# Kernel tuning notes

Measured on AMD Instinct MI355X. Metric: run time of the kernel, lower is better.

## Reference

```python
import jax, jax.numpy as jnp
import numpy as np

H = 1024        # hidden_size
V = 50257       # output_size (vocab)
L = 50          # max_length (encoder positions)
N_LAYERS = 2    # python loop count over the shared single-layer GRU


def setup_inputs() -> dict:
    key = jax.random.key(0)
    ks = jax.random.split(key, 16)
    s = 0.02
    return {
        "input_ids": jax.random.randint(ks[0], (1,), 0, V),
        "hidden": jax.random.normal(ks[1], (1, 1, H), jnp.float32),
        "encoder_outputs": jax.random.normal(ks[2], (L, H), jnp.float32),
        # learned parameters
        "emb": jax.random.normal(ks[3], (V, H), jnp.float32) * s,
        "attn_w": jax.random.normal(ks[4], (L, 2 * H), jnp.float32) * s,
        "attn_b": jnp.zeros((L,), jnp.float32),
        "comb_w": jax.random.normal(ks[5], (H, 2 * H), jnp.float32) * s,
        "comb_b": jnp.zeros((H,), jnp.float32),
        "w_ih": jax.random.normal(ks[6], (3 * H, H), jnp.float32) * s,
        "w_hh": jax.random.normal(ks[7], (3 * H, H), jnp.float32) * s,
        "b_ih": jnp.zeros((3 * H,), jnp.float32),
        "b_hh": jnp.zeros((3 * H,), jnp.float32),
        "out_w": jax.random.normal(ks[8], (V, H), jnp.float32) * s,
        "out_b": jnp.zeros((V,), jnp.float32),
    }


def _gru_cell(x, h, w_ih, w_hh, b_ih, b_hh):
    # PyTorch GRU gate order: [r, z, n] stacked along dim 0 of (3H, H) weights.
    gx = w_ih @ x + b_ih
    gh = w_hh @ h + b_hh
    r = jax.nn.sigmoid(gx[:H] + gh[:H])
    z = jax.nn.sigmoid(gx[H:2 * H] + gh[H:2 * H])
    n = jnp.tanh(gx[2 * H:] + r * gh[2 * H:])
    return (1.0 - z) * n + z * h


def reference(input_ids, hidden, encoder_outputs, emb, attn_w, attn_b,
              comb_w, comb_b, w_ih, w_hh, b_ih, b_hh, out_w, out_b):
    # batch=1 single decode step; dropout is identity (eval mode)
    embedded = emb[input_ids[0]]                     # [H]
    h = hidden[0, 0]                                 # [H]
    concat = jnp.concatenate([embedded, h])          # [2H]
    attn_weights = jax.nn.softmax(attn_w @ concat + attn_b)   # [L]
    attn_applied = attn_weights @ encoder_outputs    # [H]  (bmm with batch 1)
    output = comb_w @ jnp.concatenate([embedded, attn_applied]) + comb_b  # [H]
    for _ in range(N_LAYERS):                        # shared-weight GRU called twice
        x = jax.nn.relu(output)
        h = _gru_cell(x, h, w_ih, w_hh, b_ih, b_hh)
        output = h
    log_probs = jax.nn.log_softmax(out_w @ output + out_b)    # [V]
    return log_probs[None, :], h[None, None, :], attn_weights[None, :]
```

## Files before the change

kernel.cpp:

```cpp
#include <hip/hip_runtime.h>
#include <hip/hip_bf16.h>

#define H 1024
#define V 50257
#define L 50

__global__ void attn_kernel(const int* __restrict__ input_ids,
                            const float* __restrict__ hidden,
                            const float* __restrict__ enc,
                            const float* __restrict__ emb,
                            const float* __restrict__ attn_w,
                            const float* __restrict__ attn_b,
                            float* __restrict__ ws_emb,
                            float* __restrict__ ws_app,
                            float* __restrict__ out_attnw) {
    __shared__ __align__(16) float s_concat[2 * H];
    __shared__ float s_w[L];
    const int tid = threadIdx.x;
    const int token = input_ids[0];

    const float4* e4 = (const float4*)(emb + (size_t)token * H);
    const float4* h4 = (const float4*)hidden;
    {
        float4 e = e4[tid];
        float4 h = h4[tid];
        ((float4*)s_concat)[tid] = e;
        ((float4*)(s_concat + H))[tid] = h;
        ((float4*)ws_emb)[tid] = e;
    }
    __syncthreads();

    const int wave = tid >> 6, lane = tid & 63;
    for (int l = wave; l < L; l += 4) {
        const float4* r4 = (const float4*)(attn_w + (size_t)l * 2 * H);
        const float4* c4 = (const float4*)s_concat;
        float acc = 0.f;
        for (int k = lane; k < 512; k += 64) {
            float4 a = r4[k], b = c4[k];
            acc += a.x * b.x + a.y * b.y + a.z * b.z + a.w * b.w;
        }
        #pragma unroll
        for (int off = 32; off; off >>= 1) acc += __shfl_down(acc, off);
        if (lane == 0) s_w[l] = acc + attn_b[l];
    }
    __syncthreads();

    if (tid == 0) {
        float m = s_w[0];
        for (int l = 1; l < L; ++l) m = fmaxf(m, s_w[l]);
        float s = 0.f;
        for (int l = 0; l < L; ++l) { s_w[l] = __expf(s_w[l] - m); s += s_w[l]; }
        float inv = 1.f / s;
        for (int l = 0; l < L; ++l) s_w[l] *= inv;
    }
    __syncthreads();
    if (tid < L) out_attnw[tid] = s_w[tid];

    float4 acc = make_float4(0.f, 0.f, 0.f, 0.f);
    for (int l = 0; l < L; ++l) {
        float w = s_w[l];
        float4 v = ((const float4*)(enc + (size_t)l * H))[tid];
        acc.x += w * v.x; acc.y += w * v.y; acc.z += w * v.z; acc.w += w * v.w;
    }
    ((float4*)ws_app)[tid] = acc;
}

__global__ void comb_kernel(const float* __restrict__ comb_w,
                            const float* __restrict__ comb_b,
                            const float* __restrict__ embedded,
                            const float* __restrict__ applied,
                            float* __restrict__ x1) {
    __shared__ __align__(16) float s_c[2 * H];
    const int tid = threadIdx.x;
    ((float4*)s_c)[tid] = ((const float4*)embedded)[tid];
    ((float4*)(s_c + H))[tid] = ((const float4*)applied)[tid];
    __syncthreads();

    const int wave = tid >> 6, lane = tid & 63;
    const int i = blockIdx.x * 4 + wave;
    const float4* r4 = (const float4*)(comb_w + (size_t)i * 2 * H);
    const float4* c4 = (const float4*)s_c;
    float acc = 0.f;
    for (int k = lane; k < 512; k += 64) {
        float4 a = r4[k], b = c4[k];
        acc += a.x * b.x + a.y * b.y + a.z * b.z + a.w * b.w;
    }
    #pragma unroll
    for (int off = 32; off; off >>= 1) acc += __shfl_down(acc, off);
    if (lane == 0) x1[i] = fmaxf(acc + comb_b[i], 0.f);
}

__global__ void gru_kernel(const float* __restrict__ x,
                           const float* __restrict__ hprev,
                           const float* __restrict__ w_ih,
                           const float* __restrict__ w_hh,
                           const float* __restrict__ b_ih,
                           const float* __restrict__ b_hh,
                           float* __restrict__ h_out,
                           float* __restrict__ x_out,
                           float* __restrict__ h_copy)
{
    __shared__ __align__(16) float s_x[H];
    __shared__ __align__(16) float s_h[H];
    const int tid = threadIdx.x;
    ((float4*)s_x)[tid] = ((const float4*)x)[tid];
    ((float4*)s_h)[tid] = ((const float4*)hprev)[tid];
    __syncthreads();

    const int wave = tid >> 6, lane = tid & 63;
    const int i = blockIdx.x * 4 + wave;
    const float4* x4 = (const float4*)s_x;
    const float4* h4 = (const float4*)s_h;
    const float4* wr_x = (const float4*)(w_ih + (size_t)i * H);
    const float4* wz_x = (const float4*)(w_ih + (size_t)(H + i) * H);
    const float4* wn_x = (const float4*)(w_ih + (size_t)(2 * H + i) * H);
    const float4* wr_h = (const float4*)(w_hh + (size_t)i * H);
    const float4* wz_h = (const float4*)(w_hh + (size_t)(H + i) * H);
    const float4* wn_h = (const float4*)(w_hh + (size_t)(2 * H + i) * H);

    float ar = 0.f, az = 0.f, an = 0.f, br = 0.f, bz = 0.f, bn = 0.f;
    for (int k = lane; k < 256; k += 64) {
        float4 xv = x4[k], hv = h4[k], t;
        t = wr_x[k]; ar += t.x * xv.x + t.y * xv.y + t.z * xv.z + t.w * xv.w;
        t = wz_x[k]; az += t.x * xv.x + t.y * xv.y + t.z * xv.z + t.w * xv.w;
        t = wn_x[k]; an += t.x * xv.x + t.y * xv.y + t.z * xv.z + t.w * xv.w;
        t = wr_h[k]; br += t.x * hv.x + t.y * hv.y + t.z * hv.z + t.w * hv.w;
        t = wz_h[k]; bz += t.x * hv.x + t.y * hv.y + t.z * hv.z + t.w * hv.w;
        t = wn_h[k]; bn += t.x * hv.x + t.y * hv.y + t.z * hv.z + t.w * hv.w;
    }
    #pragma unroll
    for (int off = 32; off; off >>= 1) {
        ar += __shfl_down(ar, off); az += __shfl_down(az, off);
        an += __shfl_down(an, off); br += __shfl_down(br, off);
        bz += __shfl_down(bz, off); bn += __shfl_down(bn, off);
    }
    if (lane == 0) {
        float gxr = ar + b_ih[i],         ghr = br + b_hh[i];
        float gxz = az + b_ih[H + i],     ghz = bz + b_hh[H + i];
        float gxn = an + b_ih[2 * H + i], ghn = bn + b_hh[2 * H + i];
        float r = 1.f / (1.f + expf(-(gxr + ghr)));
        float z = 1.f / (1.f + expf(-(gxz + ghz)));
        float n = tanhf(gxn + r * ghn);
        float hn = (1.f - z) * n + z * s_h[i];
        h_out[i] = hn;
        if (x_out) x_out[i] = fmaxf(hn, 0.f);
        if (h_copy) h_copy[i] = hn;
    }
}

__global__ void logits_kernel(const float* __restrict__ out_w,
                              const float* __restrict__ out_b,
                              const float* __restrict__ h,
                              float* __restrict__ logits,
                              float* __restrict__ partials) {
    __shared__ __align__(16) float s_h[H];
    __shared__ float s_part[4];
    const int tid = threadIdx.x;
    ((float4*)s_h)[tid] = ((const float4*)h)[tid];
    __syncthreads();

    const int wave = tid >> 6, lane = tid & 63;
    const float4* h4 = (const float4*)s_h;
    float psum = 0.f;
    #pragma unroll
    for (int rr = 0; rr < 2; ++rr) {
        const int v = blockIdx.x * 8 + wave * 2 + rr;
        if (v < V) {
            const float4* w4 = (const float4*)(out_w + (size_t)v * H);
            float acc = 0.f;
            for (int k = lane; k < 256; k += 64) {
                float4 a = w4[k], b = h4[k];
                acc += a.x * b.x + a.y * b.y + a.z * b.z + a.w * b.w;
            }
            #pragma unroll
            for (int off = 32; off; off >>= 1) acc += __shfl_down(acc, off);
            if (lane == 0) {
                float lg = acc + out_b[v];
                logits[v] = lg;
                psum += expf(lg);
            }
        }
    }
    if (lane == 0) s_part[wave] = psum;
    __syncthreads();
    if (tid == 0) partials[blockIdx.x] = s_part[0] + s_part[1] + s_part[2] + s_part[3];
}

__global__ void lse_kernel(const float* __restrict__ partials, int n,
                           float* __restrict__ lse) {
    __shared__ float red[256];
    const int tid = threadIdx.x;
    float s = 0.f;
    for (int i = tid; i < n; i += 256) s += partials[i];
    red[tid] = s;
    __syncthreads();
    for (int off = 128; off; off >>= 1) {
        if (tid < off) red[tid] += red[tid + off];
        __syncthreads();
    }
    if (tid == 0) *lse = logf(red[0]);
}

__global__ void sub_kernel(const float* __restrict__ logits,
                           const float* __restrict__ lse,
                           float* __restrict__ out) {
    const int v = blockIdx.x * 256 + threadIdx.x;
    if (v < V) out[v] = logits[v] - *lse;
}

extern "C" void kernel_launch(void* const* d_in, const int* in_sizes, int n_in,
                              void* d_out, int out_size, void* d_ws, size_t ws_size,
                              hipStream_t stream) {
    const int*   input_ids = (const int*)d_in[0];
    const float* hidden    = (const float*)d_in[1];
    const float* enc       = (const float*)d_in[2];
    const float* emb       = (const float*)d_in[3];
    const float* attn_w    = (const float*)d_in[4];
    const float* attn_b    = (const float*)d_in[5];
    const float* comb_w    = (const float*)d_in[6];
    const float* comb_b    = (const float*)d_in[7];
    const float* w_ih      = (const float*)d_in[8];
    const float* w_hh      = (const float*)d_in[9];
    const float* b_ih      = (const float*)d_in[10];
    const float* b_hh      = (const float*)d_in[11];
    const float* out_w     = (const float*)d_in[12];
    const float* out_b     = (const float*)d_in[13];

    float* out = (float*)d_out;
    float* ws  = (float*)d_ws;
    float* ws_emb    = ws;
    float* ws_app    = ws + 1024;
    float* ws_x1     = ws + 2048;
    float* ws_h1     = ws + 3072;
    float* ws_x2     = ws + 4096;
    float* ws_h2     = ws + 5120;
    float* ws_logits = ws + 6144;
    float* ws_part   = ws + 6144 + 50432;
    float* ws_lse    = ws_part + 6400;

    const int nblk_logits = (V + 7) / 8;

    attn_kernel<<<1, 256, 0, stream>>>(input_ids, hidden, enc, emb, attn_w, attn_b,
                                       ws_emb, ws_app, out + V + H);
    comb_kernel<<<256, 256, 0, stream>>>(comb_w, comb_b, ws_emb, ws_app, ws_x1);
    gru_kernel<<<256, 256, 0, stream>>>(ws_x1, hidden, w_ih, w_hh, b_ih, b_hh,
                                        ws_h1, ws_x2, nullptr);
    gru_kernel<<<256, 256, 0, stream>>>(ws_x2, ws_h1, w_ih, w_hh, b_ih, b_hh,
                                        ws_h2, nullptr, out + V);
    logits_kernel<<<nblk_logits, 256, 0, stream>>>(out_w, out_b, ws_h2,
                                                   ws_logits, ws_part);
    lse_kernel<<<1, 256, 0, stream>>>(ws_part, nblk_logits, ws_lse);
    sub_kernel<<<(V + 255) / 256, 256, 0, stream>>>(ws_logits, ws_lse, out);
}
```

Baseline: 451.2 us.

## Split attention into multi-block kernels, unroll GEMV loops, write logits in place

The single-block attention kernel is split into a 50-block score kernel and a 4-block softmax-plus-weighted-sum kernel, spreading that work across more compute units. The comb, GRU and logits dot-product loops are fully unrolled, and the logits kernel interleaves loads for its two rows per wave. Logits are now written straight into the output buffer and the subtraction runs in place, dropping a workspace round trip. The split adds one more kernel launch, and every applied_kernel thread recomputes the 50-element softmax redundantly.

```diff
diff --git a/kernel.cpp b/kernel.cpp
--- a/kernel.cpp
+++ b/kernel.cpp
@@ -5,74 +5,64 @@
 #define V 50257
 #define L 50
 
-__global__ void attn_kernel(const int* __restrict__ input_ids,
-                            const float* __restrict__ hidden,
-                            const float* __restrict__ enc,
-                            const float* __restrict__ emb,
-                            const float* __restrict__ attn_w,
-                            const float* __restrict__ attn_b,
-                            float* __restrict__ ws_emb,
-                            float* __restrict__ ws_app,
-                            float* __restrict__ out_attnw) {
-    __shared__ __align__(16) float s_concat[2 * H];
-    __shared__ float s_w[L];
-    const int tid = threadIdx.x;
+__global__ void scores_kernel(const int* __restrict__ input_ids,
+                              const float* __restrict__ hidden,
+                              const float* __restrict__ emb,
+                              const float* __restrict__ attn_w,
+                              const float* __restrict__ attn_b,
+                              float* __restrict__ ws_scores) {
+    __shared__ float s_part[8];
+    const int tid = threadIdx.x;
+    const int l   = blockIdx.x;
+    const int wave = tid >> 6, lane = tid & 63;
     const int token = input_ids[0];
 
-    const float4* e4 = (const float4*)(emb + (size_t)token * H);
-    const float4* h4 = (const float4*)hidden;
-    {
-        float4 e = e4[tid];
-        float4 h = h4[tid];
-        ((float4*)s_concat)[tid] = e;
-        ((float4*)(s_concat + H))[tid] = h;
-        ((float4*)ws_emb)[tid] = e;
-    }
-    __syncthreads();
-
-    const int wave = tid >> 6, lane = tid & 63;
-    for (int l = wave; l < L; l += 4) {
-        const float4* r4 = (const float4*)(attn_w + (size_t)l * 2 * H);
-        const float4* c4 = (const float4*)s_concat;
-        float acc = 0.f;
-        for (int k = lane; k < 512; k += 64) {
-            float4 a = r4[k], b = c4[k];
-            acc += a.x * b.x + a.y * b.y + a.z * b.z + a.w * b.w;
-        }
+    float4 a = ((const float4*)(attn_w + (size_t)l * 2 * H))[tid];
+    float4 x = (tid < 256) ? ((const float4*)(emb + (size_t)token * H))[tid]
+                           : ((const float4*)hidden)[tid - 256];
+    float acc = a.x * x.x + a.y * x.y + a.z * x.z + a.w * x.w;
+    #pragma unroll
+    for (int off = 32; off; off >>= 1) acc += __shfl_down(acc, off);
+    if (lane == 0) s_part[wave] = acc;
+    __syncthreads();
+    if (tid == 0) {
+        float s = 0.f;
         #pragma unroll
-        for (int off = 32; off; off >>= 1) acc += __shfl_down(acc, off);
-        if (lane == 0) s_w[l] = acc + attn_b[l];
-    }
-    __syncthreads();
-
-    if (tid == 0) {
-        float m = s_w[0];
-        for (int l = 1; l < L; ++l) m = fmaxf(m, s_w[l]);
-        float s = 0.f;
-        for (int l = 0; l < L; ++l) { s_w[l] = __expf(s_w[l] - m); s += s_w[l]; }
-        float inv = 1.f / s;
-        for (int l = 0; l < L; ++l) s_w[l] *= inv;
-    }
-    __syncthreads();
-    if (tid < L) out_attnw[tid] = s_w[tid];
-
-    float4 acc = make_float4(0.f, 0.f, 0.f, 0.f);
-    for (int l = 0; l < L; ++l) {
-        float w = s_w[l];
-        float4 v = ((const float4*)(enc + (size_t)l * H))[tid];
-        acc.x += w * v.x; acc.y += w * v.y; acc.z += w * v.z; acc.w += w * v.w;
-    }
-    ((float4*)ws_app)[tid] = acc;
+        for (int w = 0; w < 8; ++w) s += s_part[w];
+        ws_scores[l] = s + attn_b[l];
+    }
+}
+
+__global__ void applied_kernel(const float* __restrict__ ws_scores,
+                               const float* __restrict__ enc,
+                               float* __restrict__ ws_app,
+                               float* __restrict__ out_attnw) {
+    const int j = blockIdx.x * 256 + threadIdx.x;
+    float w[L];
+    float m = ws_scores[0];
+    #pragma unroll
+    for (int l = 1; l < L; ++l) m = fmaxf(m, ws_scores[l]);
+    float s = 0.f;
+    #pragma unroll
+    for (int l = 0; l < L; ++l) { w[l] = expf(ws_scores[l] - m); s += w[l]; }
+    float inv = 1.f / s;
+    float acc = 0.f;
+    #pragma unroll
+    for (int l = 0; l < L; ++l) { w[l] *= inv; acc += w[l] * enc[l * H + j]; }
+    ws_app[j] = acc;
+    if (blockIdx.x == 0 && threadIdx.x < L) out_attnw[threadIdx.x] = w[threadIdx.x];
 }
 
 __global__ void comb_kernel(const float* __restrict__ comb_w,
                             const float* __restrict__ comb_b,
-                            const float* __restrict__ embedded,
+                            const int* __restrict__ input_ids,
+                            const float* __restrict__ emb,
                             const float* __restrict__ applied,
                             float* __restrict__ x1) {
     __shared__ __align__(16) float s_c[2 * H];
     const int tid = threadIdx.x;
-    ((float4*)s_c)[tid] = ((const float4*)embedded)[tid];
+    const int token = input_ids[0];
+    ((float4*)s_c)[tid] = ((const float4*)(emb + (size_t)token * H))[tid];
     ((float4*)(s_c + H))[tid] = ((const float4*)applied)[tid];
     __syncthreads();
 
@@ -81,7 +71,9 @@
     const float4* r4 = (const float4*)(comb_w + (size_t)i * 2 * H);
     const float4* c4 = (const float4*)s_c;
     float acc = 0.f;
-    for (int k = lane; k < 512; k += 64) {
+    #pragma unroll
+    for (int kk = 0; kk < 8; ++kk) {
+        int k = kk * 64 + lane;
         float4 a = r4[k], b = c4[k];
         acc += a.x * b.x + a.y * b.y + a.z * b.z + a.w * b.w;
     }
@@ -119,7 +111,9 @@
     const float4* wn_h = (const float4*)(w_hh + (size_t)(2 * H + i) * H);
 
     float ar = 0.f, az = 0.f, an = 0.f, br = 0.f, bz = 0.f, bn = 0.f;
-    for (int k = lane; k < 256; k += 64) {
+    #pragma unroll
+    for (int kk = 0; kk < 4; ++kk) {
+        int k = kk * 64 + lane;
         float4 xv = x4[k], hv = h4[k], t;
         t = wr_x[k]; ar += t.x * xv.x + t.y * xv.y + t.z * xv.z + t.w * xv.w;
         t = wz_x[k]; az += t.x * xv.x + t.y * xv.y + t.z * xv.z + t.w * xv.w;
@@ -143,7 +137,7 @@
         float n = tanhf(gxn + r * ghn);
         float hn = (1.f - z) * n + z * s_h[i];
         h_out[i] = hn;
-        if (x_out) x_out[i] = fmaxf(hn, 0.f);
+        if (x_out)  x_out[i]  = fmaxf(hn, 0.f);
         if (h_copy) h_copy[i] = hn;
     }
 }
@@ -151,7 +145,7 @@
 __global__ void logits_kernel(const float* __restrict__ out_w,
                               const float* __restrict__ out_b,
                               const float* __restrict__ h,
-                              float* __restrict__ logits,
+                              float* __restrict__ out,
                               float* __restrict__ partials) {
     __shared__ __align__(16) float s_h[H];
     __shared__ float s_part[4];
@@ -161,29 +155,43 @@
 
     const int wave = tid >> 6, lane = tid & 63;
     const float4* h4 = (const float4*)s_h;
+    const int v0 = blockIdx.x * 8 + wave * 2;
+    const int v1 = v0 + 1;
+    float acc0 = 0.f, acc1 = 0.f;
+    const float4* w0 = (const float4*)(out_w + (size_t)v0 * H);
+    const float4* w1 = (const float4*)(out_w + (size_t)v1 * H);
+    if (v1 < V) {
+        #pragma unroll
+        for (int kk = 0; kk < 4; ++kk) {
+            int k = kk * 64 + lane;
+            float4 b = h4[k];
+            float4 a0 = w0[k], a1 = w1[k];
+            acc0 += a0.x * b.x + a0.y * b.y + a0.z * b.z + a0.w * b.w;
+            acc1 += a1.x * b.x + a1.y * b.y + a1.z * b.z + a1.w * b.w;
+        }
+    } else if (v0 < V) {
+        #pragma unroll
+        for (int kk = 0; kk < 4; ++kk) {
+            int k = kk * 64 + lane;
+            float4 b = h4[k];
+            float4 a0 = w0[k];
+            acc0 += a0.x * b.x + a0.y * b.y + a0.z * b.z + a0.w * b.w;
+        }
+    }
+    #pragma unroll
+    for (int off = 32; off; off >>= 1) {
+        acc0 += __shfl_down(acc0, off);
+        acc1 += __shfl_down(acc1, off);
+    }
     float psum = 0.f;
-    #pragma unroll
-    for (int rr = 0; rr < 2; ++rr) {
-        const int v = blockIdx.x * 8 + wave * 2 + rr;
-        if (v < V) {
-            const float4* w4 = (const float4*)(out_w + (size_t)v * H);
-            float acc = 0.f;
-            for (int k = lane; k < 256; k += 64) {
-                float4 a = w4[k], b = h4[k];
-                acc += a.x * b.x + a.y * b.y + a.z * b.z + a.w * b.w;
-            }
-            #pragma unroll
-            for (int off = 32; off; off >>= 1) acc += __shfl_down(acc, off);
-            if (lane == 0) {
-                float lg = acc + out_b[v];
-                logits[v] = lg;
-                psum += expf(lg);
-            }
-        }
-    }
-    if (lane == 0) s_part[wave] = psum;
-    __syncthreads();
-    if (tid == 0) partials[blockIdx.x] = s_part[0] + s_part[1] + s_part[2] + s_part[3];
+    if (lane == 0) {
+        if (v0 < V) { float lg = acc0 + out_b[v0]; out[v0] = lg; psum += expf(lg); }
+        if (v1 < V) { float lg = acc1 + out_b[v1]; out[v1] = lg; psum += expf(lg); }
+        s_part[wave] = psum;
+    }
+    __syncthreads();
+    if (tid == 0)
+        partials[blockIdx.x] = s_part[0] + s_part[1] + s_part[2] + s_part[3];
 }
 
 __global__ void lse_kernel(const float* __restrict__ partials, int n,
@@ -201,11 +209,10 @@
     if (tid == 0) *lse = logf(red[0]);
 }
 
-__global__ void sub_kernel(const float* __restrict__ logits,
-                           const float* __restrict__ lse,
-                           float* __restrict__ out) {
+__global__ void sub_kernel(float* __restrict__ out,
+                           const float* __restrict__ lse) {
     const int v = blockIdx.x * 256 + threadIdx.x;
-    if (v < V) out[v] = logits[v] - *lse;
+    if (v < V) out[v] -= *lse;
 }
 
 extern "C" void kernel_launch(void* const* d_in, const int* in_sizes, int n_in,
@@ -228,27 +235,28 @@
 
     float* out = (float*)d_out;
     float* ws  = (float*)d_ws;
-    float* ws_emb    = ws;
-    float* ws_app    = ws + 1024;
-    float* ws_x1     = ws + 2048;
-    float* ws_h1     = ws + 3072;
-    float* ws_x2     = ws + 4096;
-    float* ws_h2     = ws + 5120;
-    float* ws_logits = ws + 6144;
-    float* ws_part   = ws + 6144 + 50432;
+    float* ws_scores = ws;
+    float* ws_app    = ws + 64;
+    float* ws_x1     = ws_app + H;
+    float* ws_h1     = ws_x1 + H;
+    float* ws_x2     = ws_h1 + H;
+    float* ws_h2     = ws_x2 + H;
+    float* ws_part   = ws_h2 + H;
     float* ws_lse    = ws_part + 6400;
 
     const int nblk_logits = (V + 7) / 8;
 
-    attn_kernel<<<1, 256, 0, stream>>>(input_ids, hidden, enc, emb, attn_w, attn_b,
-                                       ws_emb, ws_app, out + V + H);
-    comb_kernel<<<256, 256, 0, stream>>>(comb_w, comb_b, ws_emb, ws_app, ws_x1);
+    scores_kernel<<<L, 512, 0, stream>>>(input_ids, hidden, emb, attn_w, attn_b,
+                                         ws_scores);
+    applied_kernel<<<4, 256, 0, stream>>>(ws_scores, enc, ws_app, out + V + H);
+    comb_kernel<<<256, 256, 0, stream>>>(comb_w, comb_b, input_ids, emb, ws_app,
+                                         ws_x1);
     gru_kernel<<<256, 256, 0, stream>>>(ws_x1, hidden, w_ih, w_hh, b_ih, b_hh,
                                         ws_h1, ws_x2, nullptr);
     gru_kernel<<<256, 256, 0, stream>>>(ws_x2, ws_h1, w_ih, w_hh, b_ih, b_hh,
                                         ws_h2, nullptr, out + V);
     logits_kernel<<<nblk_logits, 256, 0, stream>>>(out_w, out_b, ws_h2,
-                                                   ws_logits, ws_part);
+                                                   out, ws_part);
     lse_kernel<<<1, 256, 0, stream>>>(ws_part, nblk_logits, ws_lse);
-    sub_kernel<<<(V + 255) / 256, 256, 0, stream>>>(ws_logits, ws_lse, out);
-}
+    sub_kernel<<<(V + 255) / 256, 256, 0, stream>>>(out, ws_lse);
+}
```

Measured after the change: 430.6 us. 1.05x faster.
